# Performance work log

Measured on AMD Instinct MI355X. Metric: run time of the kernel, lower is better.

Reference implementation:

```python
import jax, jax.numpy as jnp
import numpy as np

B, T, DL, DM, H = 8, 4096, 1024, 1024, 8
HD = min(DL, DM) // H  # 128


def setup_inputs() -> dict:
    key = jax.random.key(0)
    ks = jax.random.split(key, 8)
    s = 0.02

    def w(k, shape):
        return jax.random.normal(k, shape, jnp.float32) * s

    return {
        "liquid_repr": jax.random.normal(ks[0], (B, T, DL), jnp.float32),
        "mamba_repr": jax.random.normal(ks[1], (B, T, DM), jnp.float32),
        "Wlq": w(ks[2], (DL, H * HD)), "blq": jnp.zeros((H * HD,), jnp.float32),
        "Wmkv": w(ks[3], (DM, 2 * H * HD)), "bmkv": jnp.zeros((2 * H * HD,), jnp.float32),
        "Wmq": w(ks[4], (DM, H * HD)), "bmq": jnp.zeros((H * HD,), jnp.float32),
        "Wlkv": w(ks[5], (DL, 2 * H * HD)), "blkv": jnp.zeros((2 * H * HD,), jnp.float32),
        "Wlo": w(ks[6], (H * HD, DL)), "blo": jnp.zeros((DL,), jnp.float32),
        "Wmo": w(ks[7], (H * HD, DM)), "bmo": jnp.zeros((DM,), jnp.float32),
    }


def _attn(q, k, v):
    # q,k,v: [B,T,H,HD]. Faithful to torch: matmul over last two dims ->
    # scores [B,T,H,H] (attention over the heads axis per timestep).
    scores = jnp.einsum('bthd,btgd->bthg', q, k) / jnp.sqrt(jnp.float32(HD))
    w = jax.nn.softmax(scores, axis=-1)
    return jnp.einsum('bthg,btgd->bthd', w, v)


def reference(liquid_repr, mamba_repr, Wlq, blq, Wmkv, bmkv, Wmq, bmq,
              Wlkv, blkv, Wlo, blo, Wmo, bmo):
    b, t, _ = liquid_repr.shape
    # liquid queries mamba
    q_l = (liquid_repr @ Wlq + blq).reshape(b, t, H, HD)
    kv_m = (mamba_repr @ Wmkv + bmkv).reshape(b, t, H, 2 * HD)
    k_m, v_m = kv_m[..., :HD], kv_m[..., HD:]
    a_l = _attn(q_l, k_m, v_m).reshape(b, t, H * HD)
    enhanced_liquid = liquid_repr + a_l @ Wlo + blo
    # mamba queries liquid
    q_m = (mamba_repr @ Wmq + bmq).reshape(b, t, H, HD)
    kv_l = (liquid_repr @ Wlkv + blkv).reshape(b, t, H, 2 * HD)
    k_l, v_l = kv_l[..., :HD], kv_l[..., HD:]
    a_m = _attn(q_m, k_l, v_l).reshape(b, t, H * HD)
    enhanced_mamba = mamba_repr + a_m @ Wmo + bmo
    return enhanced_liquid, enhanced_mamba
```

## Files before the change

kernel.cpp:

```cpp
#include <hip/hip_runtime.h>

typedef unsigned short u16;
typedef unsigned int u32;

typedef __attribute__((ext_vector_type(4))) float floatx4;
typedef __attribute__((ext_vector_type(8))) __bf16 bf16x8;

typedef __attribute__((address_space(3))) u32 lds_u32_t;
typedef __attribute__((address_space(1))) u32 glb_u32_t;

__device__ __forceinline__ void gld_lds16(const u16* g, u16* l) {
    __builtin_amdgcn_global_load_lds((glb_u32_t*)g, (lds_u32_t*)l, 16, 0, 0);
}

__device__ __forceinline__ u16 f2bf(float f) {
    u32 u = __float_as_uint(f);
    u += 0x7fffu + ((u >> 16) & 1u);
    return (u16)(u >> 16);
}
__device__ __forceinline__ u32 pk2(float a, float b) {
    u32 x = __float_as_uint(a), y = __float_as_uint(b);
    x += 0x7fffu + ((x >> 16) & 1u);
    y += 0x7fffu + ((y >> 16) & 1u);
    return (x >> 16) | (y & 0xffff0000u);
}
__device__ __forceinline__ float bl(u32 u) { return __uint_as_float(u << 16); }
__device__ __forceinline__ float bh(u32 u) { return __uint_as_float(u & 0xffff0000u); }

#define SWZ(d) ((d) ^ ((((d) >> 7) & 7) << 4))

#define BM 256
#define BN 128
#define BK 64

__global__ __launch_bounds__(256) void convert2_f32_bf16(
    const float* __restrict__ s0, u16* __restrict__ d0,
    const float* __restrict__ s1, u16* __restrict__ d1)
{
    const size_t half = (size_t)16384 * 256 * 8;
    size_t i = ((size_t)blockIdx.x * 256 + threadIdx.x) * 8;
    const float* s = s0; u16* d = d0;
    if (i >= half) { i -= half; s = s1; d = d1; }
    float4 a = *(const float4*)(s + i);
    float4 b = *(const float4*)(s + i + 4);
    *(uint4*)(d + i) = make_uint4(pk2(a.x, a.y), pk2(a.z, a.w),
                                  pk2(b.x, b.y), pk2(b.z, b.w));
}

__device__ __forceinline__ void remap_bmbn(int nbn, int& bm, int& bn) {
    const int nwg = (int)gridDim.x;
    const int flat = (int)blockIdx.x;
    const int wg = (flat & 7) * (nwg >> 3) + (flat >> 3);
    bn = wg % nbn;
    bm = wg / nbn;
}

__device__ __forceinline__ void stage_tiles(
    const u16* __restrict__ A, int lda, const u16* __restrict__ Bt, int K,
    int bm, int bn, int k0, u16* sA, u16* sB, int tid)
{
#pragma unroll
    for (int j = 0; j < 8; ++j) {
        const int clin = tid + j * 256;
        const int csrc = clin ^ ((clin >> 3) & 7);
        const int r = csrc >> 3, c = (csrc & 7) * 8;
        gld_lds16(A + (size_t)(bm * BM + r) * lda + k0 + c, &sA[clin * 8]);
    }
#pragma unroll
    for (int j = 0; j < 4; ++j) {
        const int clin = tid + j * 256;
        const int csrc = clin ^ ((clin >> 3) & 7);
        const int r = csrc >> 3, c = (csrc & 7) * 8;
        gld_lds16(Bt + (size_t)(bn * BN + r) * K + k0 + c, &sB[clin * 8]);
    }
}

__global__ __launch_bounds__(256, 2) void gemm_a16_c16(
    const u16* __restrict__ A, int lda,
    const u16* __restrict__ Bt,
    const float* __restrict__ bias,
    u16* __restrict__ C, int ldc,
    int K, int nbn)
{
    __shared__ __align__(16) u16 sA[BM * BK];
    __shared__ __align__(16) u16 sB[BN * BK];
    const int tid  = threadIdx.x;
    int bm, bn; remap_bmbn(nbn, bm, bn);
    const int lane = tid & 63,  wave = tid >> 6;
    const int wm   = wave >> 1, wn   = wave & 1;
    const int l15  = lane & 15, quad = lane >> 4;
    const char* sAb = (const char*)sA;
    const char* sBb = (const char*)sB;

    floatx4 acc[8][4] = {};

    for (int k0 = 0; k0 < K; k0 += BK) {
        __syncthreads();
        stage_tiles(A, lda, Bt, K, bm, bn, k0, sA, sB, tid);
        __syncthreads();

#pragma unroll
        for (int ks = 0; ks < 2; ++ks) {
            bf16x8 af[8], bfr[4];
#pragma unroll
            for (int mi = 0; mi < 8; mi++)
                af[mi] = *(const bf16x8*)(sAb +
                    SWZ((wm * 128 + mi * 16 + l15) * 128 + ks * 64 + quad * 16));
#pragma unroll
            for (int ni = 0; ni < 4; ni++)
                bfr[ni] = *(const bf16x8*)(sBb +
                    SWZ((wn * 64 + ni * 16 + l15) * 128 + ks * 64 + quad * 16));
#pragma unroll
            for (int mi = 0; mi < 8; mi++)
#pragma unroll
                for (int ni = 0; ni < 4; ni++)
                    acc[mi][ni] = __builtin_amdgcn_mfma_f32_16x16x32_bf16(
                        af[mi], bfr[ni], acc[mi][ni], 0, 0, 0);
        }
    }

    const int row0 = bm * BM + wm * 128 + quad * 4;
    const int col0 = bn * BN + wn * 64 + l15;
#pragma unroll
    for (int mi = 0; mi < 8; mi++) {
#pragma unroll
        for (int ni = 0; ni < 4; ni++) {
            const int col = col0 + ni * 16;
            const float bv = bias[col];
#pragma unroll
            for (int r = 0; r < 4; r++) {
                const int row = row0 + mi * 16 + r;
                C[(size_t)row * ldc + col] = f2bf(acc[mi][ni][r] + bv);
            }
        }
    }
}

__global__ __launch_bounds__(256, 2) void gemm_a16_c32(
    const u16* __restrict__ A, int lda,
    const u16* __restrict__ Bt,
    const float* __restrict__ bias,
    const float* __restrict__ R, int ldr,
    float* __restrict__ C, int ldc,
    int K, int nbn)
{
    __shared__ __align__(16) u16 sA[BM * BK];
    __shared__ __align__(16) u16 sB[BN * BK];
    const int tid  = threadIdx.x;
    int bm, bn; remap_bmbn(nbn, bm, bn);
    const int lane = tid & 63,  wave = tid >> 6;
    const int wm   = wave >> 1, wn   = wave & 1;
    const int l15  = lane & 15, quad = lane >> 4;
    const char* sAb = (const char*)sA;
    const char* sBb = (const char*)sB;

    floatx4 acc[8][4] = {};

    for (int k0 = 0; k0 < K; k0 += BK) {
        __syncthreads();
        stage_tiles(A, lda, Bt, K, bm, bn, k0, sA, sB, tid);
        __syncthreads();

#pragma unroll
        for (int ks = 0; ks < 2; ++ks) {
            bf16x8 af[8], bfr[4];
#pragma unroll
            for (int mi = 0; mi < 8; mi++)
                af[mi] = *(const bf16x8*)(sAb +
                    SWZ((wm * 128 + mi * 16 + l15) * 128 + ks * 64 + quad * 16));
#pragma unroll
            for (int ni = 0; ni < 4; ni++)
                bfr[ni] = *(const bf16x8*)(sBb +
                    SWZ((wn * 64 + ni * 16 + l15) * 128 + ks * 64 + quad * 16));
#pragma unroll
            for (int mi = 0; mi < 8; mi++)
#pragma unroll
                for (int ni = 0; ni < 4; ni++)
                    acc[mi][ni] = __builtin_amdgcn_mfma_f32_16x16x32_bf16(
                        af[mi], bfr[ni], acc[mi][ni], 0, 0, 0);
        }
    }

    const int row0 = bm * BM + wm * 128 + quad * 4;
    const int col0 = bn * BN + wn * 64 + l15;
#pragma unroll
    for (int mi = 0; mi < 8; mi++) {
#pragma unroll
        for (int ni = 0; ni < 4; ni++) {
            const int col = col0 + ni * 16;
            const float bv = bias[col];
#pragma unroll
            for (int r = 0; r < 4; r++) {
                const int row = row0 + mi * 16 + r;
                C[(size_t)row * ldc + col] =
                    acc[mi][ni][r] + bv + R[(size_t)row * ldr + col];
            }
        }
    }
}

__global__ __launch_bounds__(256) void attn8(
    const u16* Q,
    const u16* __restrict__ KV,
    u16* O,
    int qstride, int kvstride)
{
    const int wid = threadIdx.x >> 6, lane = threadIdx.x & 63;
    const size_t pos = (size_t)blockIdx.x * 4 + wid;
    const u16* qrow  = Q  + pos * qstride;
    const u16* kvrow = KV + pos * kvstride;
    const int h = lane >> 3, g = lane & 7;

    const u16* qh = qrow  + h * 128;
    const u16* kg = kvrow + g * 256;
    float s0 = 0.f, s1 = 0.f, s2 = 0.f, s3 = 0.f;
#pragma unroll
    for (int j = 0; j < 16; ++j) {
        uint4 qa = *(const uint4*)(qh + j * 8);
        uint4 ka = *(const uint4*)(kg + j * 8);
        s0 += bl(qa.x) * bl(ka.x);  s1 += bh(qa.x) * bh(ka.x);
        s2 += bl(qa.y) * bl(ka.y);  s3 += bh(qa.y) * bh(ka.y);
        s0 += bl(qa.z) * bl(ka.z);  s1 += bh(qa.z) * bh(ka.z);
        s2 += bl(qa.w) * bl(ka.w);  s3 += bh(qa.w) * bh(ka.w);
    }
    float s = ((s0 + s1) + (s2 + s3)) * 0.08838834764831845f;

    float m = s;
    m = fmaxf(m, __shfl_xor(m, 1, 64));
    m = fmaxf(m, __shfl_xor(m, 2, 64));
    m = fmaxf(m, __shfl_xor(m, 4, 64));
    float p = __expf(s - m);
    float sum = p;
    sum += __shfl_xor(sum, 1, 64);
    sum += __shfl_xor(sum, 2, 64);
    sum += __shfl_xor(sum, 4, 64);
    const float w = p / sum;

    const int db = g;
    float o[16];
#pragma unroll
    for (int j = 0; j < 16; ++j) o[j] = 0.f;
    const u16* vbase = kvrow + 128 + db * 16;
#pragma unroll
    for (int gg = 0; gg < 8; ++gg) {
        const float wv = __shfl(w, h * 8 + gg, 64);
        const u16* vp = vbase + gg * 256;
        uint4 va = *(const uint4*)(vp);
        uint4 vb = *(const uint4*)(vp + 8);
        o[0]  += wv * bl(va.x);  o[1]  += wv * bh(va.x);
        o[2]  += wv * bl(va.y);  o[3]  += wv * bh(va.y);
        o[4]  += wv * bl(va.z);  o[5]  += wv * bh(va.z);
        o[6]  += wv * bl(va.w);  o[7]  += wv * bh(va.w);
        o[8]  += wv * bl(vb.x);  o[9]  += wv * bh(vb.x);
        o[10] += wv * bl(vb.y);  o[11] += wv * bh(vb.y);
        o[12] += wv * bl(vb.z);  o[13] += wv * bh(vb.z);
        o[14] += wv * bl(vb.w);  o[15] += wv * bh(vb.w);
    }

    u16* orow = O + pos * qstride + h * 128 + db * 16;
    u32 pk[8];
#pragma unroll
    for (int j = 0; j < 8; ++j)
        pk[j] = pk2(o[2 * j], o[2 * j + 1]);
    ((uint4*)orow)[0] = make_uint4(pk[0], pk[1], pk[2], pk[3]);
    ((uint4*)orow)[1] = make_uint4(pk[4], pk[5], pk[6], pk[7]);
}

__global__ __launch_bounds__(256) void transpose6_f32_bf16(
    const float* __restrict__ s0, u16* __restrict__ d0, int n0,
    const float* __restrict__ s1, u16* __restrict__ d1, int n1,
    const float* __restrict__ s2, u16* __restrict__ d2, int n2,
    const float* __restrict__ s3, u16* __restrict__ d3, int n3,
    const float* __restrict__ s4, u16* __restrict__ d4, int n4,
    const float* __restrict__ s5, u16* __restrict__ d5, int n5)
{
    const float* srcs[6] = {s0, s1, s2, s3, s4, s5};
    u16*         dsts[6] = {d0, d1, d2, d3, d4, d5};
    const int    ns[6]   = {n0, n1, n2, n3, n4, n5};
    const int z = blockIdx.z;
    const int N = ns[z];
    const int c0 = blockIdx.x * 32;
    if (c0 >= N) return;
    const float* src = srcs[z];
    u16* dst = dsts[z];
    const int K = 1024;
    __shared__ float tile[32][33];
    const int tx = threadIdx.x & 31, ty = threadIdx.x >> 5;
    const int r0 = blockIdx.y * 32;
#pragma unroll
    for (int i = 0; i < 4; i++)
        tile[ty + i * 8][tx] = src[(size_t)(r0 + ty + i * 8) * N + c0 + tx];
    __syncthreads();
#pragma unroll
    for (int i = 0; i < 4; i++)
        dst[(size_t)(c0 + ty + i * 8) * K + r0 + tx] = f2bf(tile[tx][ty + i * 8]);
}

extern "C" void kernel_launch(void* const* d_in, const int* in_sizes, int n_in,
                              void* d_out, int out_size, void* d_ws, size_t ws_size,
                              hipStream_t stream) {
    const float* liquid = (const float*)d_in[0];
    const float* mamba  = (const float*)d_in[1];
    const float* Wlq  = (const float*)d_in[2];
    const float* blq  = (const float*)d_in[3];
    const float* Wmkv = (const float*)d_in[4];
    const float* bmkv = (const float*)d_in[5];
    const float* Wmq  = (const float*)d_in[6];
    const float* bmq  = (const float*)d_in[7];
    const float* Wlkv = (const float*)d_in[8];
    const float* blkv = (const float*)d_in[9];
    const float* Wlo  = (const float*)d_in[10];
    const float* blo  = (const float*)d_in[11];
    const float* Wmo  = (const float*)d_in[12];
    const float* bmo  = (const float*)d_in[13];
    float* out = (float*)d_out;

    u16* p = (u16*)d_ws;
    u16* WtLq  = p; p += (size_t)1024 * 1024;
    u16* WtLkv = p; p += (size_t)2048 * 1024;
    u16* WtMq  = p; p += (size_t)1024 * 1024;
    u16* WtMkv = p; p += (size_t)2048 * 1024;
    u16* WtLo  = p; p += (size_t)1024 * 1024;
    u16* WtMo  = p; p += (size_t)1024 * 1024;
    u16* Q  = p; p += (size_t)32768 * 1024;
    u16* KV = p;

    u16* Lb = (u16*)(out + (size_t)32768 * 1024);
    u16* Mb = Lb + (size_t)32768 * 1024;

    transpose6_f32_bf16<<<dim3(64, 32, 6), 256, 0, stream>>>(
        Wlq,  WtLq,  1024,
        Wlkv, WtLkv, 2048,
        Wmq,  WtMq,  1024,
        Wmkv, WtMkv, 2048,
        Wlo,  WtLo,  1024,
        Wmo,  WtMo,  1024);

    convert2_f32_bf16<<<32768, 256, 0, stream>>>(liquid, Lb, mamba, Mb);

    gemm_a16_c16<<<1024, 256, 0, stream>>>(Lb, 1024, WtLq,  blq,  Q,  1024, 1024, 8);
    gemm_a16_c16<<<2048, 256, 0, stream>>>(Mb, 1024, WtMkv, bmkv, KV, 2048, 1024, 16);
    attn8<<<8192, 256, 0, stream>>>(Q, KV, Q, 1024, 2048);
    gemm_a16_c32<<<1024, 256, 0, stream>>>(Q, 1024, WtLo, blo, liquid, 1024,
                                           out, 1024, 1024, 8);

    gemm_a16_c16<<<1024, 256, 0, stream>>>(Mb, 1024, WtMq,  bmq,  Q,  1024, 1024, 8);
    gemm_a16_c16<<<2048, 256, 0, stream>>>(Lb, 1024, WtLkv, blkv, KV, 2048, 1024, 16);
    attn8<<<8192, 256, 0, stream>>>(Q, KV, Q, 1024, 2048);
    gemm_a16_c32<<<1024, 256, 0, stream>>>(Q, 1024, WtMo, bmo, mamba, 1024,
                                           out + (size_t)32768 * 1024, 1024, 1024, 8);
}
```

Baseline: 1.309 ms.

## Double-buffer GEMM LDS tiles with async prefetch and shrink tile to 128x128

Both bf16 GEMM kernels now use a 128x128 tile with two LDS buffers. The next K-slice is prefetched via global_load_lds while the current one is read, synchronised with explicit vmcnt/lgkmcnt waits and s_barrier. The aim is to hide global-load latency behind MFMA work, and to give a larger grid with fewer accumulators per wave. In exchange, each tile reuses data less, so global and L2 traffic per FLOP goes up.

```diff
diff --git a/kernel.cpp b/kernel.cpp
--- a/kernel.cpp
+++ b/kernel.cpp
@@ -27,9 +27,14 @@
 __device__ __forceinline__ float bl(u32 u) { return __uint_as_float(u << 16); }
 __device__ __forceinline__ float bh(u32 u) { return __uint_as_float(u & 0xffff0000u); }
 
+#define BARRIER() asm volatile("s_barrier" ::: "memory")
+#define WAITVM8() asm volatile("s_waitcnt vmcnt(8)" ::: "memory")
+#define WAITVM0() asm volatile("s_waitcnt vmcnt(0)" ::: "memory")
+#define WAITLGKM0() asm volatile("s_waitcnt lgkmcnt(0)" ::: "memory")
+
 #define SWZ(d) ((d) ^ ((((d) >> 7) & 7) << 4))
 
-#define BM 256
+#define BM 128
 #define BN 128
 #define BK 64
 
@@ -55,23 +60,23 @@
     bm = wg / nbn;
 }
 
-__device__ __forceinline__ void stage_tiles(
+__device__ __forceinline__ void stage128(
     const u16* __restrict__ A, int lda, const u16* __restrict__ Bt, int K,
-    int bm, int bn, int k0, u16* sA, u16* sB, int tid)
-{
-#pragma unroll
-    for (int j = 0; j < 8; ++j) {
-        const int clin = tid + j * 256;
-        const int csrc = clin ^ ((clin >> 3) & 7);
-        const int r = csrc >> 3, c = (csrc & 7) * 8;
-        gld_lds16(A + (size_t)(bm * BM + r) * lda + k0 + c, &sA[clin * 8]);
-    }
+    int bm, int bn, int k0, u16* buf, int tid)
+{
 #pragma unroll
     for (int j = 0; j < 4; ++j) {
         const int clin = tid + j * 256;
         const int csrc = clin ^ ((clin >> 3) & 7);
         const int r = csrc >> 3, c = (csrc & 7) * 8;
-        gld_lds16(Bt + (size_t)(bn * BN + r) * K + k0 + c, &sB[clin * 8]);
+        gld_lds16(A + (size_t)(bm * BM + r) * lda + k0 + c, &buf[clin * 8]);
+    }
+#pragma unroll
+    for (int j = 0; j < 4; ++j) {
+        const int clin = tid + j * 256;
+        const int csrc = clin ^ ((clin >> 3) & 7);
+        const int r = csrc >> 3, c = (csrc & 7) * 8;
+        gld_lds16(Bt + (size_t)(bn * BN + r) * K + k0 + c, &buf[8192 + clin * 8]);
     }
 }
 
@@ -82,47 +87,59 @@
     u16* __restrict__ C, int ldc,
     int K, int nbn)
 {
-    __shared__ __align__(16) u16 sA[BM * BK];
-    __shared__ __align__(16) u16 sB[BN * BK];
+    __shared__ __align__(16) u16 lds[32768];
     const int tid  = threadIdx.x;
     int bm, bn; remap_bmbn(nbn, bm, bn);
     const int lane = tid & 63,  wave = tid >> 6;
     const int wm   = wave >> 1, wn   = wave & 1;
     const int l15  = lane & 15, quad = lane >> 4;
-    const char* sAb = (const char*)sA;
-    const char* sBb = (const char*)sB;
-
-    floatx4 acc[8][4] = {};
-
-    for (int k0 = 0; k0 < K; k0 += BK) {
-        __syncthreads();
-        stage_tiles(A, lda, Bt, K, bm, bn, k0, sA, sB, tid);
-        __syncthreads();
-
+
+    floatx4 acc[4][4] = {};
+    const int NT = K >> 6;
+
+    stage128(A, lda, Bt, K, bm, bn, 0, lds, tid);
+
+    for (int t = 0; t < NT; ++t) {
+        const int cur = t & 1;
+        if (t + 1 < NT) {
+            stage128(A, lda, Bt, K, bm, bn, (t + 1) * BK, lds + (cur ^ 1) * 16384, tid);
+            WAITVM8();
+        } else {
+            WAITVM0();
+        }
+        BARRIER();
+
+        const char* sAb = (const char*)lds + cur * 32768;
+        const char* sBb = sAb + 16384;
+        bf16x8 af[2][4], bq[2][4];
 #pragma unroll
         for (int ks = 0; ks < 2; ++ks) {
-            bf16x8 af[8], bfr[4];
-#pragma unroll
-            for (int mi = 0; mi < 8; mi++)
-                af[mi] = *(const bf16x8*)(sAb +
-                    SWZ((wm * 128 + mi * 16 + l15) * 128 + ks * 64 + quad * 16));
+#pragma unroll
+            for (int mi = 0; mi < 4; mi++)
+                af[ks][mi] = *(const bf16x8*)(sAb +
+                    SWZ((wm * 64 + mi * 16 + l15) * 128 + ks * 64 + quad * 16));
 #pragma unroll
             for (int ni = 0; ni < 4; ni++)
-                bfr[ni] = *(const bf16x8*)(sBb +
+                bq[ks][ni] = *(const bf16x8*)(sBb +
                     SWZ((wn * 64 + ni * 16 + l15) * 128 + ks * 64 + quad * 16));
-#pragma unroll
-            for (int mi = 0; mi < 8; mi++)
+        }
+        WAITLGKM0();
+        BARRIER();
+
+#pragma unroll
+        for (int ks = 0; ks < 2; ++ks)
+#pragma unroll
+            for (int mi = 0; mi < 4; mi++)
 #pragma unroll
                 for (int ni = 0; ni < 4; ni++)
                     acc[mi][ni] = __builtin_amdgcn_mfma_f32_16x16x32_bf16(
-                        af[mi], bfr[ni], acc[mi][ni], 0, 0, 0);
-        }
-    }
-
-    const int row0 = bm * BM + wm * 128 + quad * 4;
+                        af[ks][mi], bq[ks][ni], acc[mi][ni], 0, 0, 0);
+    }
+
+    const int row0 = bm * BM + wm * 64 + quad * 4;
     const int col0 = bn * BN + wn * 64 + l15;
 #pragma unroll
-    for (int mi = 0; mi < 8; mi++) {
+    for (int mi = 0; mi < 4; mi++) {
 #pragma unroll
         for (int ni = 0; ni < 4; ni++) {
             const int col = col0 + ni * 16;
@@ -144,47 +161,59 @@
     float* __restrict__ C, int ldc,
     int K, int nbn)
 {
-    __shared__ __align__(16) u16 sA[BM * BK];
-    __shared__ __align__(16) u16 sB[BN * BK];
+    __shared__ __align__(16) u16 lds[32768];
     const int tid  = threadIdx.x;
     int bm, bn; remap_bmbn(nbn, bm, bn);
     const int lane = tid & 63,  wave = tid >> 6;
     const int wm   = wave >> 1, wn   = wave & 1;
     const int l15  = lane & 15, quad = lane >> 4;
-    const char* sAb = (const char*)sA;
-    const char* sBb = (const char*)sB;
-
-    floatx4 acc[8][4] = {};
-
-    for (int k0 = 0; k0 < K; k0 += BK) {
-        __syncthreads();
-        stage_tiles(A, lda, Bt, K, bm, bn, k0, sA, sB, tid);
-        __syncthreads();
-
+
+    floatx4 acc[4][4] = {};
+    const int NT = K >> 6;
+
+    stage128(A, lda, Bt, K, bm, bn, 0, lds, tid);
+
+    for (int t = 0; t < NT; ++t) {
+        const int cur = t & 1;
+        if (t + 1 < NT) {
+            stage128(A, lda, Bt, K, bm, bn, (t + 1) * BK, lds + (cur ^ 1) * 16384, tid);
+            WAITVM8();
+        } else {
+            WAITVM0();
+        }
+        BARRIER();
+
+        const char* sAb = (const char*)lds + cur * 32768;
+        const char* sBb = sAb + 16384;
+        bf16x8 af[2][4], bq[2][4];
 #pragma unroll
         for (int ks = 0; ks < 2; ++ks) {
-            bf16x8 af[8], bfr[4];
-#pragma unroll
-            for (int mi = 0; mi < 8; mi++)
-                af[mi] = *(const bf16x8*)(sAb +
-                    SWZ((wm * 128 + mi * 16 + l15) * 128 + ks * 64 + quad * 16));
+#pragma unroll
+            for (int mi = 0; mi < 4; mi++)
+                af[ks][mi] = *(const bf16x8*)(sAb +
+                    SWZ((wm * 64 + mi * 16 + l15) * 128 + ks * 64 + quad * 16));
 #pragma unroll
             for (int ni = 0; ni < 4; ni++)
-                bfr[ni] = *(const bf16x8*)(sBb +
+                bq[ks][ni] = *(const bf16x8*)(sBb +
                     SWZ((wn * 64 + ni * 16 + l15) * 128 + ks * 64 + quad * 16));
-#pragma unroll
-            for (int mi = 0; mi < 8; mi++)
+        }
+        WAITLGKM0();
+        BARRIER();
+
+#pragma unroll
+        for (int ks = 0; ks < 2; ++ks)
+#pragma unroll
+            for (int mi = 0; mi < 4; mi++)
 #pragma unroll
                 for (int ni = 0; ni < 4; ni++)
                     acc[mi][ni] = __builtin_amdgcn_mfma_f32_16x16x32_bf16(
-                        af[mi], bfr[ni], acc[mi][ni], 0, 0, 0);
-        }
-    }
-
-    const int row0 = bm * BM + wm * 128 + quad * 4;
+                        af[ks][mi], bq[ks][ni], acc[mi][ni], 0, 0, 0);
+    }
+
+    const int row0 = bm * BM + wm * 64 + quad * 4;
     const int col0 = bn * BN + wn * 64 + l15;
 #pragma unroll
-    for (int mi = 0; mi < 8; mi++) {
+    for (int mi = 0; mi < 4; mi++) {
 #pragma unroll
         for (int ni = 0; ni < 4; ni++) {
             const int col = col0 + ni * 16;
@@ -338,15 +367,15 @@
 
     convert2_f32_bf16<<<32768, 256, 0, stream>>>(liquid, Lb, mamba, Mb);
 
-    gemm_a16_c16<<<1024, 256, 0, stream>>>(Lb, 1024, WtLq,  blq,  Q,  1024, 1024, 8);
-    gemm_a16_c16<<<2048, 256, 0, stream>>>(Mb, 1024, WtMkv, bmkv, KV, 2048, 1024, 16);
+    gemm_a16_c16<<<2048, 256, 0, stream>>>(Lb, 1024, WtLq,  blq,  Q,  1024, 1024, 8);
+    gemm_a16_c16<<<4096, 256, 0, stream>>>(Mb, 1024, WtMkv, bmkv, KV, 2048, 1024, 16);
     attn8<<<8192, 256, 0, stream>>>(Q, KV, Q, 1024, 2048);
-    gemm_a16_c32<<<1024, 256, 0, stream>>>(Q, 1024, WtLo, blo, liquid, 1024,
+    gemm_a16_c32<<<2048, 256, 0, stream>>>(Q, 1024, WtLo, blo, liquid, 1024,
                                            out, 1024, 1024, 8);
 
-    gemm_a16_c16<<<1024, 256, 0, stream>>>(Mb, 1024, WtMq,  bmq,  Q,  1024, 1024, 8);
-    gemm_a16_c16<<<2048, 256, 0, stream>>>(Lb, 1024, WtLkv, blkv, KV, 2048, 1024, 16);
+    gemm_a16_c16<<<2048, 256, 0, stream>>>(Mb, 1024, WtMq,  bmq,  Q,  1024, 1024, 8);
+    gemm_a16_c16<<<4096, 256, 0, stream>>>(Lb, 1024, WtLkv, blkv, KV, 2048, 1024, 16);
     attn8<<<8192, 256, 0, stream>>>(Q, KV, Q, 1024, 2048);
-    gemm_a16_c32<<<1024, 256, 0, stream>>>(Q, 1024, WtMo, bmo, mamba, 1024,
+    gemm_a16_c32<<<2048, 256, 0, stream>>>(Q, 1024, WtMo, bmo, mamba, 1024,
                                            out + (size_t)32768 * 1024, 1024, 1024, 8);
 }
```

After: 1.319 ms. Within noise of the previous version (+0.8%).
